# Kernel optimization log

Measured on AMD Instinct MI355X. Metric: run time of the kernel, lower is better.

Reference implementation:

```python
import jax, jax.numpy as jnp
import numpy as np

B, L, E = 512, 64, 1024
D_MODEL, H = 1024, 16
HD = D_MODEL // H  # 64
SMOL_CH, SMOL_HID, SMOL_GEN = 32, 256, 256
LN_EPS = 1e-3


def _layernorm(x, g, b, eps=LN_EPS):
    m = jnp.mean(x, axis=-1, keepdims=True)
    v = jnp.mean(jnp.square(x - m), axis=-1, keepdims=True)
    return (x - m) * jax.lax.rsqrt(v + eps) * g + b


def setup_inputs() -> dict:
    key = jax.random.key(0)
    ks = jax.random.split(key, 12)
    s = lambda fan_in: 1.0 / np.sqrt(fan_in)
    inp = {
        'x': jax.random.normal(ks[0], (B, L, E), dtype=jnp.float32),
        # attention projections (stored as [in, out])
        'wq': jax.random.normal(ks[1], (E, D_MODEL), dtype=jnp.float32) * s(E),
        'bq': jnp.zeros((D_MODEL,), jnp.float32),
        'wk': jax.random.normal(ks[2], (E, D_MODEL), dtype=jnp.float32) * s(E),
        'bk': jnp.zeros((D_MODEL,), jnp.float32),
        'wv': jax.random.normal(ks[3], (E, D_MODEL), dtype=jnp.float32) * s(E),
        'bv': jnp.zeros((D_MODEL,), jnp.float32),
        'wo': jax.random.normal(ks[4], (D_MODEL, E), dtype=jnp.float32) * s(D_MODEL),
        'bo': jnp.zeros((E,), jnp.float32),
        # smolgen hypernetwork
        'sc_w': jax.random.normal(ks[5], (E, SMOL_CH), dtype=jnp.float32) * s(E),
        'sh1_w': jax.random.normal(ks[6], (L * SMOL_CH, SMOL_HID), dtype=jnp.float32) * s(L * SMOL_CH),
        'sh1_b': jnp.zeros((SMOL_HID,), jnp.float32),
        'ln1_g': jnp.ones((SMOL_HID,), jnp.float32),
        'ln1_b': jnp.zeros((SMOL_HID,), jnp.float32),
        'sg_w': jax.random.normal(ks[7], (SMOL_HID, H * SMOL_GEN), dtype=jnp.float32) * s(SMOL_HID),
        'sg_b': jnp.zeros((H * SMOL_GEN,), jnp.float32),
        'ln2_g': jnp.ones((H * SMOL_GEN,), jnp.float32),
        'ln2_b': jnp.zeros((H * SMOL_GEN,), jnp.float32),
        'swg_w': jax.random.normal(ks[8], (SMOL_GEN, L * L), dtype=jnp.float32) * s(SMOL_GEN),
    }
    return inp


def reference(x, wq, bq, wk, bk, wv, bv, wo, bo,
              sc_w, sh1_w, sh1_b, ln1_g, ln1_b,
              sg_w, sg_b, ln2_g, ln2_b, swg_w):
    b, l, _ = x.shape
    # q/k/v projections -> [b, h, l, hd]
    q = (x @ wq + bq).reshape(b, l, H, HD).transpose(0, 2, 1, 3)
    k = (x @ wk + bk).reshape(b, l, H, HD).transpose(0, 2, 1, 3)
    v = (x @ wv + bv).reshape(b, l, H, HD).transpose(0, 2, 1, 3)

    scale = jnp.sqrt(jnp.asarray(HD, x.dtype))
    attn_logits = jnp.einsum('bhqd,bhkd->bhqk', q, k) / scale  # [b,h,l,l]

    # smolgen: per-batch, per-head additive bias on the logits
    compressed = (x @ sc_w).reshape(b, l * SMOL_CH)            # [b, 2048]
    hidden = _layernorm(jax.nn.silu(compressed @ sh1_w + sh1_b), ln1_g, ln1_b)
    gen = _layernorm(jax.nn.silu(hidden @ sg_w + sg_b), ln2_g, ln2_b)
    gen = gen.reshape(b, H, SMOL_GEN)
    smol_w = (gen @ swg_w).reshape(b, H, l, l)
    attn_logits = attn_logits + smol_w

    # manual numerically-stable softmax (as in source)
    attn_logits = attn_logits - jnp.max(attn_logits, axis=-1, keepdims=True)
    attn_weights = jnp.exp(attn_logits)
    attn_weights = attn_weights / jnp.sum(attn_weights, axis=-1, keepdims=True)

    attn_output = jnp.einsum('bhqk,bhkd->bhqd', attn_weights, v)
    attn_output = attn_output.transpose(0, 2, 1, 3).reshape(b, l, D_MODEL)
    return attn_output @ wo + bo
```

## Files before the change

kernel.cpp:

```cpp
#include <hip/hip_runtime.h>
#include <hip/hip_bf16.h>

typedef unsigned short u16;
typedef __attribute__((ext_vector_type(8))) short short8;
typedef __attribute__((ext_vector_type(4))) float f32x4;
typedef const __attribute__((address_space(1))) void GV;
typedef __attribute__((address_space(3))) void LV;
#define GLOAD16(g, l) __builtin_amdgcn_global_load_lds((GV*)(g), (LV*)(l), 16, 0, 0)
#define BAR() asm volatile("s_barrier" ::: "memory")

#define BATCH 512
#define LSEQ  64
#define EMB   1024
#define NH    16
#define NQKV  3328
#define MROWS (BATCH*LSEQ)

__device__ __forceinline__ u16 f2b(float f){
  __hip_bfloat16 h = __float2bfloat16(f);
  return *reinterpret_cast<u16*>(&h);
}
__device__ __forceinline__ float b2f(u16 u){
  return __uint_as_float(((unsigned)u) << 16);
}
__device__ __forceinline__ uint2 pack4(float4 v){
  unsigned lo = (unsigned)f2b(v.x) | ((unsigned)f2b(v.y) << 16);
  unsigned hi = (unsigned)f2b(v.z) | ((unsigned)f2b(v.w) << 16);
  return make_uint2(lo, hi);
}

__device__ __forceinline__ void tpose(const float* __restrict__ src, u16* __restrict__ dst,
                                      int K, int N, int dstLd, int dstRowOff,
                                      int blk, int tid, float (*t)[33]){
  int nbx = N >> 5;
  int bx = blk % nbx, by = blk / nbx;
  int n0 = bx << 5, k0 = by << 5;
  int lx = tid & 31, ly = tid >> 5;
  #pragma unroll
  for (int i = 0; i < 32; i += 8)
    t[ly + i][lx] = src[(size_t)(k0 + ly + i) * N + n0 + lx];
  __syncthreads();
  #pragma unroll
  for (int i = 0; i < 32; i += 8)
    dst[(size_t)(dstRowOff + n0 + ly + i) * dstLd + k0 + lx] = f2b(t[lx][ly + i]);
}

#define PREP_BLOCKS 38157
__global__ __launch_bounds__(256) void prep_all(const float* __restrict__ x, u16* __restrict__ xb,
                                                const float* __restrict__ wq, const float* __restrict__ wk,
                                                const float* __restrict__ wv, const float* __restrict__ sc_w,
                                                const float* __restrict__ wo, const float* __restrict__ swg_w,
                                                u16* __restrict__ wqkvT, u16* __restrict__ woT,
                                                u16* __restrict__ swgT,
                                                const float* __restrict__ bq, const float* __restrict__ bk,
                                                const float* __restrict__ bv, float* __restrict__ qbias){
  __shared__ float t[32][33];
  const int blk = blockIdx.x, tid = threadIdx.x;
  if (blk < 32768){
    size_t i = ((size_t)blk * 256 + tid) * 4;
    float4 v = *(const float4*)&x[i];
    *(uint2*)&xb[i] = pack4(v);
  } else if (blk < 33792){
    tpose(wq,   wqkvT, 1024, 1024, 1024, 0,    blk - 32768, tid, t);
  } else if (blk < 34816){
    tpose(wk,   wqkvT, 1024, 1024, 1024, 1024, blk - 33792, tid, t);
  } else if (blk < 35840){
    tpose(wv,   wqkvT, 1024, 1024, 1024, 2048, blk - 34816, tid, t);
  } else if (blk < 35872){
    tpose(sc_w, wqkvT, 1024, 32,   1024, 3072, blk - 35840, tid, t);
  } else if (blk < 36896){
    tpose(wo,   woT,   1024, 1024, 1024, 0,    blk - 35872, tid, t);
  } else if (blk < 37920){
    tpose(swg_w, swgT, 256,  4096, 256,  0,    blk - 36896, tid, t);
  } else if (blk < 38144){
    size_t i = (size_t)(blk - 37920) * 1024 + tid * 4;
    *(uint2*)&wqkvT[(size_t)3104 * 1024 + i] = make_uint2(0, 0);
  } else {
    int i = (blk - 38144) * 256 + tid;
    if (i < NQKV){
      float v = 0.f;
      if (i < 1024) v = bq[i];
      else if (i < 2048) v = bk[i - 1024];
      else if (i < 3072) v = bv[i - 2048];
      qbias[i] = v;
    }
  }
}

template<int OUT_BF16, int HAS_BIAS>
__global__ __launch_bounds__(512, 2) void gemm256(const u16* __restrict__ A,
                                                  const u16* __restrict__ Bt,
                                                  const float* __restrict__ bias,
                                                  void* __restrict__ Cv,
                                                  int M, int N, int K){
  __shared__ u16 lA[2][16384];
  __shared__ u16 lB[2][16384];
  const int ntn = N >> 8;
  const int nwg = gridDim.x, bid = blockIdx.x;
  const int qq = nwg >> 3, r8 = nwg & 7, xcd = bid & 7, kk = bid >> 3;
  const int wg = (xcd < r8 ? xcd * (qq + 1) : r8 * (qq + 1) + (xcd - r8) * qq) + kk;
  const int tm = wg / ntn, tn = wg % ntn;
  const int m0 = tm << 8, n0 = tn << 8;
  const int tid = threadIdx.x;
  const int w = tid >> 6, lane = tid & 63;
  const int wm = w >> 2, wn = w & 3;
  const int l15 = lane & 15, l4 = lane >> 4;

  size_t ga[2][2], gb[2][2];
  #pragma unroll
  for (int j = 0; j < 2; j++){
    int ci = w * 128 + j * 64 + lane;
    int rh = ci >> 3, s = ci & 7;
    int gk = (s ^ (rh & 7)) * 8;
    #pragma unroll
    for (int h = 0; h < 2; h++){
      ga[h][j] = (size_t)(m0 + h * 128 + rh) * K + gk;
      gb[h][j] = (size_t)(n0 + h * 128 + rh) * K + gk;
    }
  }
  const int nk = K >> 6;

  auto stA = [&](int buf, int h, int kt){
    #pragma unroll
    for (int j = 0; j < 2; j++)
      GLOAD16(A + ga[h][j] + (size_t)kt * 64, &lA[buf][h * 8192 + (w * 128 + j * 64) * 8]);
  };
  auto stB = [&](int buf, int h, int kt){
    #pragma unroll
    for (int j = 0; j < 2; j++)
      GLOAD16(Bt + gb[h][j] + (size_t)kt * 64, &lB[buf][h * 8192 + (w * 128 + j * 64) * 8]);
  };

  stA(0, 0, 0); stB(0, 0, 0); stB(0, 1, 0); stA(0, 1, 0);
  stA(1, 0, 1); stB(1, 0, 1); stB(1, 1, 1);
  asm volatile("s_waitcnt vmcnt(6)" ::: "memory");
  BAR();

  f32x4 acc[8][4] = {};
  short8 a[4][2], b[4][2];

  for (int t = 0; t < nk; ++t){
    const int cur = t & 1;
    const u16* la = lA[cur];
    const u16* lb = lB[cur];

    #pragma unroll
    for (int f = 0; f < 4; f++){
      int r = f * 32 + wm * 16 + l15;
      #pragma unroll
      for (int ks = 0; ks < 2; ks++){
        int c = ks * 4 + l4;
        a[f][ks] = *(const short8*)&la[r * 64 + ((c ^ (r & 7)) * 8)];
      }
    }
    #pragma unroll
    for (int g = 0; g < 2; g++){
      int r = g * 64 + wn * 16 + l15;
      #pragma unroll
      for (int ks = 0; ks < 2; ks++){
        int c = ks * 4 + l4;
        b[g][ks] = *(const short8*)&lb[r * 64 + ((c ^ (r & 7)) * 8)];
      }
    }
    if (t + 1 < nk) stA(cur ^ 1, 1, t + 1);
    BAR();
    __builtin_amdgcn_s_setprio(1);
    #pragma unroll
    for (int f = 0; f < 4; f++)
      #pragma unroll
      for (int g = 0; g < 2; g++)
        #pragma unroll
        for (int ks = 0; ks < 2; ks++)
          acc[f][g] = __builtin_amdgcn_mfma_f32_16x16x32_bf16(a[f][ks], b[g][ks], acc[f][g], 0, 0, 0);
    __builtin_amdgcn_s_setprio(0);
    BAR();

    #pragma unroll
    for (int g = 2; g < 4; g++){
      int r = (g - 2) * 64 + wn * 16 + l15;
      #pragma unroll
      for (int ks = 0; ks < 2; ks++){
        int c = ks * 4 + l4;
        b[g][ks] = *(const short8*)&lb[8192 + r * 64 + ((c ^ (r & 7)) * 8)];
      }
    }
    if (t + 2 < nk) stA(cur, 0, t + 2);
    BAR();
    __builtin_amdgcn_s_setprio(1);
    #pragma unroll
    for (int f = 0; f < 4; f++)
      #pragma unroll
      for (int g = 2; g < 4; g++)
        #pragma unroll
        for (int ks = 0; ks < 2; ks++)
          acc[f][g] = __builtin_amdgcn_mfma_f32_16x16x32_bf16(a[f][ks], b[g][ks], acc[f][g], 0, 0, 0);
    __builtin_amdgcn_s_setprio(0);
    BAR();

    #pragma unroll
    for (int f = 0; f < 4; f++){
      int r = f * 32 + wm * 16 + l15;
      #pragma unroll
      for (int ks = 0; ks < 2; ks++){
        int c = ks * 4 + l4;
        a[f][ks] = *(const short8*)&la[8192 + r * 64 + ((c ^ (r & 7)) * 8)];
      }
    }
    if (t + 2 < nk) stB(cur, 0, t + 2);
    BAR();
    __builtin_amdgcn_s_setprio(1);
    #pragma unroll
    for (int f = 0; f < 4; f++)
      #pragma unroll
      for (int g = 2; g < 4; g++)
        #pragma unroll
        for (int ks = 0; ks < 2; ks++)
          acc[f + 4][g] = __builtin_amdgcn_mfma_f32_16x16x32_bf16(a[f][ks], b[g][ks], acc[f + 4][g], 0, 0, 0);
    __builtin_amdgcn_s_setprio(0);
    BAR();

    if (t + 2 < nk) stB(cur, 1, t + 2);
    if (t + 1 < nk){
      if (t + 2 < nk) asm volatile("s_waitcnt vmcnt(6)" ::: "memory");
      else            asm volatile("s_waitcnt vmcnt(0)" ::: "memory");
    }
    BAR();
    __builtin_amdgcn_s_setprio(1);
    #pragma unroll
    for (int f = 0; f < 4; f++)
      #pragma unroll
      for (int g = 0; g < 2; g++)
        #pragma unroll
        for (int ks = 0; ks < 2; ks++)
          acc[f + 4][g] = __builtin_amdgcn_mfma_f32_16x16x32_bf16(a[f][ks], b[g][ks], acc[f + 4][g], 0, 0, 0);
    __builtin_amdgcn_s_setprio(0);
    BAR();
  }

  #pragma unroll
  for (int f = 0; f < 8; f++){
    #pragma unroll
    for (int g = 0; g < 4; g++){
      int col = n0 + g * 64 + wn * 16 + l15;
      float bv = HAS_BIAS ? bias[col] : 0.0f;
      #pragma unroll
      for (int j = 0; j < 4; j++){
        int row = m0 + f * 32 + wm * 16 + l4 * 4 + j;
        float v = acc[f][g][j] + bv;
        if (OUT_BF16) ((u16*)Cv)[(size_t)row * N + col] = f2b(v);
        else          ((float*)Cv)[(size_t)row * N + col] = v;
      }
    }
  }
}

__global__ __launch_bounds__(512) void smol_hidden(const u16* __restrict__ qkvb,
                                                   const float* __restrict__ sh1_w,
                                                   const float* __restrict__ sh1_b,
                                                   const float* __restrict__ ln1_g,
                                                   const float* __restrict__ ln1_b,
                                                   float* __restrict__ hidden){
  const int b0 = blockIdx.x * 2;
  const int tid = threadIdx.x;
  __shared__ u16 cb[2][2048];
  __shared__ float part[8][2][256];
  __shared__ float rs[16];
  {
    int bi = tid >> 8, rem = tid & 255;
    int l = rem >> 2, cc = rem & 3;
    *(short8*)&cb[bi][rem * 8] =
        *(const short8*)&qkvb[(size_t)((b0 + bi) * 64 + l) * NQKV + 3072 + cc * 8];
  }
  __syncthreads();
  const int g = tid >> 6;
  const int c4 = (tid & 63) * 4;
  float4 a0 = {0,0,0,0}, a1 = {0,0,0,0};
  for (int kk2 = 0; kk2 < 256; kk2++){
    int k = g * 256 + kk2;
    float4 wv = *(const float4*)&sh1_w[(size_t)k * 256 + c4];
    float x0 = b2f(cb[0][k]), x1 = b2f(cb[1][k]);
    a0.x += x0 * wv.x; a0.y += x0 * wv.y; a0.z += x0 * wv.z; a0.w += x0 * wv.w;
    a1.x += x1 * wv.x; a1.y += x1 * wv.y; a1.z += x1 * wv.z; a1.w += x1 * wv.w;
  }
  *(float4*)&part[g][0][c4] = a0;
  *(float4*)&part[g][1][c4] = a1;
  __syncthreads();
  const int bi = tid >> 8, col = tid & 255;
  float y = sh1_b[col];
  #pragma unroll
  for (int g2 = 0; g2 < 8; g2++) y += part[g2][bi][col];
  y = y / (1.f + __expf(-y));
  float s = y, q = y * y;
  #pragma unroll
  for (int o = 32; o > 0; o >>= 1){ s += __shfl_down(s, o); q += __shfl_down(q, o); }
  int wv_ = tid >> 6;
  if ((tid & 63) == 0){ rs[wv_ * 2] = s; rs[wv_ * 2 + 1] = q; }
  __syncthreads();
  float S = 0, Q = 0;
  #pragma unroll
  for (int w2 = 0; w2 < 4; w2++){ S += rs[(bi * 4 + w2) * 2]; Q += rs[(bi * 4 + w2) * 2 + 1]; }
  float m = S * (1.f / 256.f), var = Q * (1.f / 256.f) - m * m;
  hidden[(size_t)(b0 + bi) * 256 + col] =
      (y - m) * rsqrtf(var + 1e-3f) * ln1_g[col] + ln1_b[col];
}

__global__ __launch_bounds__(512) void smol_gen(const float* __restrict__ hidden,
                                                const float* __restrict__ sg_w,
                                                const float* __restrict__ sg_b,
                                                const float* __restrict__ ln2_g,
                                                const float* __restrict__ ln2_b,
                                                u16* __restrict__ genb){
  const int b0 = blockIdx.x * 2;
  const int tid = threadIdx.x;
  __shared__ float hb[2][256];
  __shared__ float rs[32];
  if (tid < 512) hb[tid >> 8][tid & 255] = hidden[(size_t)(b0 + (tid >> 8)) * 256 + (tid & 255)];
  __syncthreads();
  const int c4 = tid * 4;
  float4 A00 = {0,0,0,0}, A01 = {0,0,0,0}, A10 = {0,0,0,0}, A11 = {0,0,0,0};
  for (int k = 0; k < 256; k++){
    float h0 = hb[0][k], h1 = hb[1][k];
    float4 w0 = *(const float4*)&sg_w[(size_t)k * 4096 + c4];
    float4 w1 = *(const float4*)&sg_w[(size_t)k * 4096 + 2048 + c4];
    A00.x += h0 * w0.x; A00.y += h0 * w0.y; A00.z += h0 * w0.z; A00.w += h0 * w0.w;
    A01.x += h0 * w1.x; A01.y += h0 * w1.y; A01.z += h0 * w1.z; A01.w += h0 * w1.w;
    A10.x += h1 * w0.x; A10.y += h1 * w0.y; A10.z += h1 * w0.z; A10.w += h1 * w0.w;
    A11.x += h1 * w1.x; A11.y += h1 * w1.y; A11.z += h1 * w1.z; A11.w += h1 * w1.w;
  }
  float4 b0v = *(const float4*)&sg_b[c4];
  float4 b1v = *(const float4*)&sg_b[2048 + c4];
  float s0 = 0, q0 = 0, s1 = 0, q1 = 0;
  float* p;
  #pragma unroll
  for (int e = 0; e < 4; e++){
    p = (float*)&A00; float y = p[e] + ((float*)&b0v)[e]; y = y / (1.f + __expf(-y)); p[e] = y; s0 += y; q0 += y * y;
    p = (float*)&A01; y = p[e] + ((float*)&b1v)[e]; y = y / (1.f + __expf(-y)); p[e] = y; s0 += y; q0 += y * y;
    p = (float*)&A10; y = p[e] + ((float*)&b0v)[e]; y = y / (1.f + __expf(-y)); p[e] = y; s1 += y; q1 += y * y;
    p = (float*)&A11; y = p[e] + ((float*)&b1v)[e]; y = y / (1.f + __expf(-y)); p[e] = y; s1 += y; q1 += y * y;
  }
  #pragma unroll
  for (int o = 32; o > 0; o >>= 1){
    s0 += __shfl_down(s0, o); q0 += __shfl_down(q0, o);
    s1 += __shfl_down(s1, o); q1 += __shfl_down(q1, o);
  }
  int wv_ = tid >> 6;
  if ((tid & 63) == 0){ rs[wv_ * 4] = s0; rs[wv_ * 4 + 1] = q0; rs[wv_ * 4 + 2] = s1; rs[wv_ * 4 + 3] = q1; }
  __syncthreads();
  float S0 = 0, Q0 = 0, S1 = 0, Q1 = 0;
  #pragma unroll
  for (int w2 = 0; w2 < 8; w2++){
    S0 += rs[w2 * 4]; Q0 += rs[w2 * 4 + 1]; S1 += rs[w2 * 4 + 2]; Q1 += rs[w2 * 4 + 3];
  }
  float m0 = S0 * (1.f / 4096.f), v0 = Q0 * (1.f / 4096.f) - m0 * m0;
  float m1 = S1 * (1.f / 4096.f), v1 = Q1 * (1.f / 4096.f) - m1 * m1;
  float is0 = rsqrtf(v0 + 1e-3f), is1 = rsqrtf(v1 + 1e-3f);
  float4 g0 = *(const float4*)&ln2_g[c4],        gb0 = *(const float4*)&ln2_b[c4];
  float4 g1 = *(const float4*)&ln2_g[2048 + c4], gb1 = *(const float4*)&ln2_b[2048 + c4];
  float4 o00, o01, o10, o11;
  #pragma unroll
  for (int e = 0; e < 4; e++){
    ((float*)&o00)[e] = (((float*)&A00)[e] - m0) * is0 * ((float*)&g0)[e] + ((float*)&gb0)[e];
    ((float*)&o01)[e] = (((float*)&A01)[e] - m0) * is0 * ((float*)&g1)[e] + ((float*)&gb1)[e];
    ((float*)&o10)[e] = (((float*)&A10)[e] - m1) * is1 * ((float*)&g0)[e] + ((float*)&gb0)[e];
    ((float*)&o11)[e] = (((float*)&A11)[e] - m1) * is1 * ((float*)&g1)[e] + ((float*)&gb1)[e];
  }
  *(uint2*)&genb[(size_t)(b0    ) * 4096 + c4]        = pack4(o00);
  *(uint2*)&genb[(size_t)(b0    ) * 4096 + 2048 + c4] = pack4(o01);
  *(uint2*)&genb[(size_t)(b0 + 1) * 4096 + c4]        = pack4(o10);
  *(uint2*)&genb[(size_t)(b0 + 1) * 4096 + 2048 + c4] = pack4(o11);
}

__global__ __launch_bounds__(256) void attn_fused(const u16* __restrict__ qkvb,
                                                  const u16* __restrict__ smolb,
                                                  u16* __restrict__ aout){
  const int bh = blockIdx.x;
  const int b = bh >> 4, h = bh & 15;
  __shared__ u16 qs[4096], kts[4096], vts[4096], ps[4096];
  const int tid = threadIdx.x, w = tid >> 6, lane = tid & 63;
  const int l15 = lane & 15, g = lane >> 4;

  const u16* qb = qkvb + (size_t)(b * 64) * NQKV + h * 64;
  const u16* kb = qb + 1024;
  const u16* vb = qb + 2048;

  #pragma unroll
  for (int i = 0; i < 2; i++){
    int c = i * 256 + tid;
    int r = c >> 3, cc = c & 7;
    int pc = cc ^ (r & 7);
    *(short8*)&qs [r * 64 + pc * 8] = *(const short8*)&qb[(size_t)r * NQKV + cc * 8];
    *(short8*)&kts[r * 64 + pc * 8] = *(const short8*)&kb[(size_t)r * NQKV + cc * 8];
    short8 vv = *(const short8*)&vb[(size_t)r * NQKV + cc * 8];
    #pragma unroll
    for (int j = 0; j < 8; j++){
      int hd = cc * 8 + j;
      int pcv = (r >> 3) ^ (hd & 7);
      vts[hd * 64 + pcv * 8 + (r & 7)] = (u16)vv[j];
    }
  }
  __syncthreads();

  f32x4 sacc[4] = {};
  #pragma unroll
  for (int ksi = 0; ksi < 2; ksi++){
    int ra = w * 16 + l15;
    int ca = ksi * 4 + g;
    short8 af = *(const short8*)&qs[ra * 64 + ((ca ^ (ra & 7)) * 8)];
    #pragma unroll
    for (int fn = 0; fn < 4; fn++){
      int rb = fn * 16 + l15;
      short8 bf = *(const short8*)&kts[rb * 64 + ((ca ^ (rb & 7)) * 8)];
      sacc[fn] = __builtin_amdgcn_mfma_f32_16x16x32_bf16(af, bf, sacc[fn], 0, 0, 0);
    }
  }

  const u16* sm = smolb + (size_t)bh * 4096;
  float vals[4][4];
  float mx[4] = {-3.4e38f, -3.4e38f, -3.4e38f, -3.4e38f};
  #pragma unroll
  for (int fn = 0; fn < 4; fn++)
    #pragma unroll
    for (int j = 0; j < 4; j++){
      int q = w * 16 + g * 4 + j;
      float v = sacc[fn][j] * 0.125f + b2f(sm[q * 64 + fn * 16 + l15]);
      vals[fn][j] = v;
      mx[j] = fmaxf(mx[j], v);
    }
  #pragma unroll
  for (int o = 1; o < 16; o <<= 1)
    #pragma unroll
    for (int j = 0; j < 4; j++) mx[j] = fmaxf(mx[j], __shfl_xor(mx[j], o));
  float sum[4] = {0, 0, 0, 0};
  #pragma unroll
  for (int fn = 0; fn < 4; fn++)
    #pragma unroll
    for (int j = 0; j < 4; j++){
      vals[fn][j] = __expf(vals[fn][j] - mx[j]);
      sum[j] += vals[fn][j];
    }
  #pragma unroll
  for (int o = 1; o < 16; o <<= 1)
    #pragma unroll
    for (int j = 0; j < 4; j++) sum[j] += __shfl_xor(sum[j], o);
  float rinv[4];
  #pragma unroll
  for (int j = 0; j < 4; j++) rinv[j] = 1.f / sum[j];

  #pragma unroll
  for (int fn = 0; fn < 4; fn++)
    #pragma unroll
    for (int j = 0; j < 4; j++){
      int q = w * 16 + g * 4 + j;
      int c = fn * 16 + l15;
      int cs = (c & 7) | ((((c >> 3) ^ (q & 7)) & 7) << 3);
      ps[q * 64 + cs] = f2b(vals[fn][j] * rinv[j]);
    }
  __syncthreads();

  f32x4 oacc[4] = {};
  #pragma unroll
  for (int ksi = 0; ksi < 2; ksi++){
    int ra = w * 16 + l15;
    int ca = ksi * 4 + g;
    short8 af = *(const short8*)&ps[ra * 64 + ((ca ^ (ra & 7)) * 8)];
    #pragma unroll
    for (int fn = 0; fn < 4; fn++){
      int rb = fn * 16 + l15;
      short8 bf = *(const short8*)&vts[rb * 64 + ((ca ^ (rb & 7)) * 8)];
      oacc[fn] = __builtin_amdgcn_mfma_f32_16x16x32_bf16(af, bf, oacc[fn], 0, 0, 0);
    }
  }
  #pragma unroll
  for (int fn = 0; fn < 4; fn++)
    #pragma unroll
    for (int j = 0; j < 4; j++){
      int q  = w * 16 + g * 4 + j;
      int hd = fn * 16 + l15;
      aout[(size_t)(b * 64 + q) * 1024 + h * 64 + hd] = f2b(oacc[fn][j]);
    }
}

extern "C" void kernel_launch(void* const* d_in, const int* in_sizes, int n_in,
                              void* d_out, int out_size, void* d_ws, size_t ws_size,
                              hipStream_t stream){
  const float* x     = (const float*)d_in[0];
  const float* wq    = (const float*)d_in[1];
  const float* bq    = (const float*)d_in[2];
  const float* wk    = (const float*)d_in[3];
  const float* bk    = (const float*)d_in[4];
  const float* wv    = (const float*)d_in[5];
  const float* bv    = (const float*)d_in[6];
  const float* wo    = (const float*)d_in[7];
  const float* bo    = (const float*)d_in[8];
  const float* sc_w  = (const float*)d_in[9];
  const float* sh1_w = (const float*)d_in[10];
  const float* sh1_b = (const float*)d_in[11];
  const float* ln1_g = (const float*)d_in[12];
  const float* ln1_b = (const float*)d_in[13];
  const float* sg_w  = (const float*)d_in[14];
  const float* sg_b  = (const float*)d_in[15];
  const float* ln2_g = (const float*)d_in[16];
  const float* ln2_b = (const float*)d_in[17];
  const float* swg_w = (const float*)d_in[18];

  char* ws = (char*)d_ws;
  size_t off = 0;
  auto alloc = [&](size_t bytes){ void* p = ws + off; off += (bytes + 255) & ~(size_t)255; return p; };
  u16*   xb    = (u16*)  alloc((size_t)MROWS * EMB * 2);
  u16*   wqkvT = (u16*)  alloc((size_t)NQKV * EMB * 2);
  float* qbias = (float*)alloc((size_t)NQKV * 4);
  u16*   woT   = (u16*)  alloc((size_t)1024 * 1024 * 2);
  u16*   swgT  = (u16*)  alloc((size_t)4096 * 256 * 2);
  u16*   qkvb  = (u16*)  alloc((size_t)MROWS * NQKV * 2);
  float* hid   = (float*)alloc((size_t)512 * 256 * 4);
  u16*   genb  = (u16*)  alloc((size_t)512 * 4096 * 2);
  u16*   smolb = (u16*)  alloc((size_t)8192 * 4096 * 2);
  u16*   aout  = (u16*)  alloc((size_t)MROWS * 1024 * 2);

  prep_all<<<PREP_BLOCKS, 256, 0, stream>>>(x, xb, wq, wk, wv, sc_w, wo, swg_w,
                                            wqkvT, woT, swgT, bq, bk, bv, qbias);

  gemm256<1, 1><<<(MROWS / 256) * (NQKV / 256), 512, 0, stream>>>(
      xb, wqkvT, qbias, qkvb, MROWS, NQKV, 1024);

  smol_hidden<<<BATCH / 2, 512, 0, stream>>>(qkvb, sh1_w, sh1_b, ln1_g, ln1_b, hid);
  smol_gen   <<<BATCH / 2, 512, 0, stream>>>(hid, sg_w, sg_b, ln2_g, ln2_b, genb);
  gemm256<1, 0><<<(8192 / 256) * (4096 / 256), 512, 0, stream>>>(
      genb, swgT, nullptr, smolb, 8192, 4096, 256);

  attn_fused<<<BATCH * NH, 256, 0, stream>>>(qkvb, smolb, aout);

  gemm256<0, 1><<<(MROWS / 256) * (1024 / 256), 512, 0, stream>>>(
      aout, woT, bo, d_out, MROWS, 1024, 1024);
}
```

Before: 782.5 us.

## Fuse smolgen hidden and gen kernels, use bf16 weights, async Q/K LDS loads

```diff
diff --git a/kernel.cpp b/kernel.cpp
--- a/kernel.cpp
+++ b/kernel.cpp
@@ -45,7 +45,7 @@
     dst[(size_t)(dstRowOff + n0 + ly + i) * dstLd + k0 + lx] = f2b(t[lx][ly + i]);
 }
 
-#define PREP_BLOCKS 38157
+#define PREP_BLOCKS 39693
 __global__ __launch_bounds__(256) void prep_all(const float* __restrict__ x, u16* __restrict__ xb,
                                                 const float* __restrict__ wq, const float* __restrict__ wk,
                                                 const float* __restrict__ wv, const float* __restrict__ sc_w,
@@ -53,7 +53,9 @@
                                                 u16* __restrict__ wqkvT, u16* __restrict__ woT,
                                                 u16* __restrict__ swgT,
                                                 const float* __restrict__ bq, const float* __restrict__ bk,
-                                                const float* __restrict__ bv, float* __restrict__ qbias){
+                                                const float* __restrict__ bv, float* __restrict__ qbias,
+                                                const float* __restrict__ sh1_w, u16* __restrict__ sh1_wb,
+                                                const float* __restrict__ sg_w,  u16* __restrict__ sg_wb){
   __shared__ float t[32][33];
   const int blk = blockIdx.x, tid = threadIdx.x;
   if (blk < 32768){
@@ -75,7 +77,7 @@
   } else if (blk < 38144){
     size_t i = (size_t)(blk - 37920) * 1024 + tid * 4;
     *(uint2*)&wqkvT[(size_t)3104 * 1024 + i] = make_uint2(0, 0);
-  } else {
+  } else if (blk < 38157){
     int i = (blk - 38144) * 256 + tid;
     if (i < NQKV){
       float v = 0.f;
@@ -84,6 +86,12 @@
       else if (i < 3072) v = bv[i - 2048];
       qbias[i] = v;
     }
+  } else if (blk < 38669){
+    size_t i = (size_t)(blk - 38157) * 1024 + tid * 4;
+    *(uint2*)&sh1_wb[i] = pack4(*(const float4*)&sh1_w[i]);
+  } else {
+    size_t i = (size_t)(blk - 38669) * 1024 + tid * 4;
+    *(uint2*)&sg_wb[i] = pack4(*(const float4*)&sg_w[i]);
   }
 }
 
@@ -254,17 +262,22 @@
   }
 }
 
-__global__ __launch_bounds__(512) void smol_hidden(const u16* __restrict__ qkvb,
-                                                   const float* __restrict__ sh1_w,
-                                                   const float* __restrict__ sh1_b,
-                                                   const float* __restrict__ ln1_g,
-                                                   const float* __restrict__ ln1_b,
-                                                   float* __restrict__ hidden){
+__global__ __launch_bounds__(512) void smol_fused(const u16* __restrict__ qkvb,
+                                                  const u16* __restrict__ sh1_wb,
+                                                  const float* __restrict__ sh1_b,
+                                                  const float* __restrict__ ln1_g,
+                                                  const float* __restrict__ ln1_b,
+                                                  const u16* __restrict__ sg_wb,
+                                                  const float* __restrict__ sg_b,
+                                                  const float* __restrict__ ln2_g,
+                                                  const float* __restrict__ ln2_b,
+                                                  u16* __restrict__ genb){
   const int b0 = blockIdx.x * 2;
   const int tid = threadIdx.x;
   __shared__ u16 cb[2][2048];
   __shared__ float part[8][2][256];
-  __shared__ float rs[16];
+  __shared__ float rs[32];
+  __shared__ float hb[2][256];
   {
     int bi = tid >> 8, rem = tid & 255;
     int l = rem >> 2, cc = rem & 3;
@@ -272,60 +285,53 @@
         *(const short8*)&qkvb[(size_t)((b0 + bi) * 64 + l) * NQKV + 3072 + cc * 8];
   }
   __syncthreads();
-  const int g = tid >> 6;
-  const int c4 = (tid & 63) * 4;
-  float4 a0 = {0,0,0,0}, a1 = {0,0,0,0};
-  for (int kk2 = 0; kk2 < 256; kk2++){
-    int k = g * 256 + kk2;
-    float4 wv = *(const float4*)&sh1_w[(size_t)k * 256 + c4];
-    float x0 = b2f(cb[0][k]), x1 = b2f(cb[1][k]);
-    a0.x += x0 * wv.x; a0.y += x0 * wv.y; a0.z += x0 * wv.z; a0.w += x0 * wv.w;
-    a1.x += x1 * wv.x; a1.y += x1 * wv.y; a1.z += x1 * wv.z; a1.w += x1 * wv.w;
-  }
-  *(float4*)&part[g][0][c4] = a0;
-  *(float4*)&part[g][1][c4] = a1;
-  __syncthreads();
-  const int bi = tid >> 8, col = tid & 255;
-  float y = sh1_b[col];
-  #pragma unroll
-  for (int g2 = 0; g2 < 8; g2++) y += part[g2][bi][col];
-  y = y / (1.f + __expf(-y));
-  float s = y, q = y * y;
-  #pragma unroll
-  for (int o = 32; o > 0; o >>= 1){ s += __shfl_down(s, o); q += __shfl_down(q, o); }
-  int wv_ = tid >> 6;
-  if ((tid & 63) == 0){ rs[wv_ * 2] = s; rs[wv_ * 2 + 1] = q; }
-  __syncthreads();
-  float S = 0, Q = 0;
-  #pragma unroll
-  for (int w2 = 0; w2 < 4; w2++){ S += rs[(bi * 4 + w2) * 2]; Q += rs[(bi * 4 + w2) * 2 + 1]; }
-  float m = S * (1.f / 256.f), var = Q * (1.f / 256.f) - m * m;
-  hidden[(size_t)(b0 + bi) * 256 + col] =
-      (y - m) * rsqrtf(var + 1e-3f) * ln1_g[col] + ln1_b[col];
-}
-
-__global__ __launch_bounds__(512) void smol_gen(const float* __restrict__ hidden,
-                                                const float* __restrict__ sg_w,
-                                                const float* __restrict__ sg_b,
-                                                const float* __restrict__ ln2_g,
-                                                const float* __restrict__ ln2_b,
-                                                u16* __restrict__ genb){
-  const int b0 = blockIdx.x * 2;
-  const int tid = threadIdx.x;
-  __shared__ float hb[2][256];
-  __shared__ float rs[32];
-  if (tid < 512) hb[tid >> 8][tid & 255] = hidden[(size_t)(b0 + (tid >> 8)) * 256 + (tid & 255)];
+  {
+    const int g = tid >> 6;
+    const int c4 = (tid & 63) * 4;
+    float4 a0 = {0,0,0,0}, a1 = {0,0,0,0};
+    for (int kk2 = 0; kk2 < 256; kk2++){
+      int k = g * 256 + kk2;
+      ushort4 wv = *(const ushort4*)&sh1_wb[(size_t)k * 256 + c4];
+      float w0 = b2f(wv.x), w1 = b2f(wv.y), w2 = b2f(wv.z), w3 = b2f(wv.w);
+      float x0 = b2f(cb[0][k]), x1 = b2f(cb[1][k]);
+      a0.x += x0 * w0; a0.y += x0 * w1; a0.z += x0 * w2; a0.w += x0 * w3;
+      a1.x += x1 * w0; a1.y += x1 * w1; a1.z += x1 * w2; a1.w += x1 * w3;
+    }
+    *(float4*)&part[g][0][c4] = a0;
+    *(float4*)&part[g][1][c4] = a1;
+  }
+  __syncthreads();
+  {
+    const int bi = tid >> 8, col = tid & 255;
+    float y = sh1_b[col];
+    #pragma unroll
+    for (int g2 = 0; g2 < 8; g2++) y += part[g2][bi][col];
+    y = y / (1.f + __expf(-y));
+    float s = y, q = y * y;
+    #pragma unroll
+    for (int o = 32; o > 0; o >>= 1){ s += __shfl_down(s, o); q += __shfl_down(q, o); }
+    int wv_ = tid >> 6;
+    if ((tid & 63) == 0){ rs[wv_ * 2] = s; rs[wv_ * 2 + 1] = q; }
+    __syncthreads();
+    float S = 0, Q = 0;
+    #pragma unroll
+    for (int w2 = 0; w2 < 4; w2++){ S += rs[(bi * 4 + w2) * 2]; Q += rs[(bi * 4 + w2) * 2 + 1]; }
+    float m = S * (1.f / 256.f), var = Q * (1.f / 256.f) - m * m;
+    hb[bi][col] = (y - m) * rsqrtf(var + 1e-3f) * ln1_g[col] + ln1_b[col];
+  }
   __syncthreads();
   const int c4 = tid * 4;
   float4 A00 = {0,0,0,0}, A01 = {0,0,0,0}, A10 = {0,0,0,0}, A11 = {0,0,0,0};
   for (int k = 0; k < 256; k++){
     float h0 = hb[0][k], h1 = hb[1][k];
-    float4 w0 = *(const float4*)&sg_w[(size_t)k * 4096 + c4];
-    float4 w1 = *(const float4*)&sg_w[(size_t)k * 4096 + 2048 + c4];
-    A00.x += h0 * w0.x; A00.y += h0 * w0.y; A00.z += h0 * w0.z; A00.w += h0 * w0.w;
-    A01.x += h0 * w1.x; A01.y += h0 * w1.y; A01.z += h0 * w1.z; A01.w += h0 * w1.w;
-    A10.x += h1 * w0.x; A10.y += h1 * w0.y; A10.z += h1 * w0.z; A10.w += h1 * w0.w;
-    A11.x += h1 * w1.x; A11.y += h1 * w1.y; A11.z += h1 * w1.z; A11.w += h1 * w1.w;
+    ushort4 u0 = *(const ushort4*)&sg_wb[(size_t)k * 4096 + c4];
+    ushort4 u1 = *(const ushort4*)&sg_wb[(size_t)k * 4096 + 2048 + c4];
+    float w00 = b2f(u0.x), w01 = b2f(u0.y), w02 = b2f(u0.z), w03 = b2f(u0.w);
+    float w10 = b2f(u1.x), w11 = b2f(u1.y), w12 = b2f(u1.z), w13 = b2f(u1.w);
+    A00.x += h0 * w00; A00.y += h0 * w01; A00.z += h0 * w02; A00.w += h0 * w03;
+    A01.x += h0 * w10; A01.y += h0 * w11; A01.z += h0 * w12; A01.w += h0 * w13;
+    A10.x += h1 * w00; A10.y += h1 * w01; A10.z += h1 * w02; A10.w += h1 * w03;
+    A11.x += h1 * w10; A11.y += h1 * w11; A11.z += h1 * w12; A11.w += h1 * w13;
   }
   float4 b0v = *(const float4*)&sg_b[c4];
   float4 b1v = *(const float4*)&sg_b[2048 + c4];
@@ -344,6 +350,7 @@
     s1 += __shfl_down(s1, o); q1 += __shfl_down(q1, o);
   }
   int wv_ = tid >> 6;
+  __syncthreads();
   if ((tid & 63) == 0){ rs[wv_ * 4] = s0; rs[wv_ * 4 + 1] = q0; rs[wv_ * 4 + 2] = s1; rs[wv_ * 4 + 3] = q1; }
   __syncthreads();
   float S0 = 0, Q0 = 0, S1 = 0, Q1 = 0;
@@ -383,13 +390,20 @@
   const u16* kb = qb + 1024;
   const u16* vb = qb + 2048;
 
+  {
+    int ci = w * 128 + lane;
+    int r = ci >> 3, s = ci & 7;
+    const u16* qsrc = qb + (size_t)r * NQKV + (s ^ (r & 7)) * 8;
+    const u16* ksrc = kb + (size_t)r * NQKV + (s ^ (r & 7)) * 8;
+    GLOAD16(qsrc,                    &qs [(w * 128) * 8]);
+    GLOAD16(qsrc + (size_t)8 * NQKV, &qs [(w * 128 + 64) * 8]);
+    GLOAD16(ksrc,                    &kts[(w * 128) * 8]);
+    GLOAD16(ksrc + (size_t)8 * NQKV, &kts[(w * 128 + 64) * 8]);
+  }
   #pragma unroll
   for (int i = 0; i < 2; i++){
     int c = i * 256 + tid;
     int r = c >> 3, cc = c & 7;
-    int pc = cc ^ (r & 7);
-    *(short8*)&qs [r * 64 + pc * 8] = *(const short8*)&qb[(size_t)r * NQKV + cc * 8];
-    *(short8*)&kts[r * 64 + pc * 8] = *(const short8*)&kb[(size_t)r * NQKV + cc * 8];
     short8 vv = *(const short8*)&vb[(size_t)r * NQKV + cc * 8];
     #pragma unroll
     for (int j = 0; j < 8; j++){
@@ -506,25 +520,27 @@
   char* ws = (char*)d_ws;
   size_t off = 0;
   auto alloc = [&](size_t bytes){ void* p = ws + off; off += (bytes + 255) & ~(size_t)255; return p; };
-  u16*   xb    = (u16*)  alloc((size_t)MROWS * EMB * 2);
-  u16*   wqkvT = (u16*)  alloc((size_t)NQKV * EMB * 2);
-  float* qbias = (float*)alloc((size_t)NQKV * 4);
-  u16*   woT   = (u16*)  alloc((size_t)1024 * 1024 * 2);
-  u16*   swgT  = (u16*)  alloc((size_t)4096 * 256 * 2);
-  u16*   qkvb  = (u16*)  alloc((size_t)MROWS * NQKV * 2);
-  float* hid   = (float*)alloc((size_t)512 * 256 * 4);
-  u16*   genb  = (u16*)  alloc((size_t)512 * 4096 * 2);
-  u16*   smolb = (u16*)  alloc((size_t)8192 * 4096 * 2);
-  u16*   aout  = (u16*)  alloc((size_t)MROWS * 1024 * 2);
+  u16*   xb     = (u16*)  alloc((size_t)MROWS * EMB * 2);
+  u16*   wqkvT  = (u16*)  alloc((size_t)NQKV * EMB * 2);
+  float* qbias  = (float*)alloc((size_t)NQKV * 4);
+  u16*   woT    = (u16*)  alloc((size_t)1024 * 1024 * 2);
+  u16*   swgT   = (u16*)  alloc((size_t)4096 * 256 * 2);
+  u16*   sh1_wb = (u16*)  alloc((size_t)2048 * 256 * 2);
+  u16*   sg_wb  = (u16*)  alloc((size_t)256 * 4096 * 2);
+  u16*   qkvb   = (u16*)  alloc((size_t)MROWS * NQKV * 2);
+  u16*   genb   = (u16*)  alloc((size_t)512 * 4096 * 2);
+  u16*   smolb  = (u16*)  alloc((size_t)8192 * 4096 * 2);
+  u16*   aout   = (u16*)  alloc((size_t)MROWS * 1024 * 2);
 
   prep_all<<<PREP_BLOCKS, 256, 0, stream>>>(x, xb, wq, wk, wv, sc_w, wo, swg_w,
-                                            wqkvT, woT, swgT, bq, bk, bv, qbias);
+                                            wqkvT, woT, swgT, bq, bk, bv, qbias,
+                                            sh1_w, sh1_wb, sg_w, sg_wb);
 
   gemm256<1, 1><<<(MROWS / 256) * (NQKV / 256), 512, 0, stream>>>(
       xb, wqkvT, qbias, qkvb, MROWS, NQKV, 1024);
 
-  smol_hidden<<<BATCH / 2, 512, 0, stream>>>(qkvb, sh1_w, sh1_b, ln1_g, ln1_b, hid);
-  smol_gen   <<<BATCH / 2, 512, 0, stream>>>(hid, sg_w, sg_b, ln2_g, ln2_b, genb);
+  smol_fused<<<BATCH / 2, 512, 0, stream>>>(qkvb, sh1_wb, sh1_b, ln1_g, ln1_b,
+                                            sg_wb, sg_b, ln2_g, ln2_b, genb);
   gemm256<1, 0><<<(8192 / 256) * (4096 / 256), 512, 0, stream>>>(
       genb, swgT, nullptr, smolb, 8192, 4096, 256);
 
```

Result: slower. 807.7 us (+3.2%).
